# Optimization experiments

Measured on AMD Instinct MI355X. Metric: run time of the kernel, lower is better.

## Reference

```python
import jax, jax.numpy as jnp
import numpy as np

BS, D_IN, D_OUT, N_MASKS = 1024, 512, 512, 8

def setup_inputs() -> dict:
    key = jax.random.key(0)
    k1, k2, k3, k4 = jax.random.split(key, 4)
    x = jax.random.normal(k1, (BS, D_IN), dtype=jnp.float32)
    state = jax.random.randint(k2, (BS,), 0, N_MASKS, dtype=jnp.int32)
    # glorot-uniform-like kernel
    limit = float(np.sqrt(6.0 / (D_IN + D_OUT)))
    kernel = jax.random.uniform(k3, (D_IN, D_OUT), dtype=jnp.float32, minval=-limit, maxval=limit)
    # binary MADE connectivity masks (0/1)
    masks = (jax.random.uniform(k4, (N_MASKS, D_IN, D_OUT)) < 0.5).astype(jnp.float32)
    return {"x": x, "state": state, "kernel": kernel, "masks": masks}

def reference(x, state, kernel, masks):
    # Math of original: out = relu(x[b] @ (kernel * masks[state[b]]))
    # Efficient form: precompute all n masked kernels (small n), batched matmul,
    # then gather per-sample result. Avoids materializing [bs, d_in, d_out].
    masked = kernel[None, :, :] * masks            # [n, d_in, d_out]
    y_all = jnp.einsum('bi,nio->bno', x, masked)   # [bs, n, d_out]
    y = jnp.take_along_axis(y_all, state[:, None, None].astype(jnp.int32), axis=1)[:, 0, :]
    return jax.nn.relu(y)
```

## Files before the change

### kernel.cpp

```cpp
#include <hip/hip_runtime.h>

#define BS 1024
#define D_IN 512
#define D_OUT 512
#define N_MASKS 8

typedef short bf16x8 __attribute__((ext_vector_type(8)));
typedef float f32x4 __attribute__((ext_vector_type(4)));

#define WF_OFF_USH (8192 / 2)
#define WF_USH     (N_MASKS * 16 * 32 * 512)
#define XB_OFF_USH (WF_OFF_USH + WF_USH)

__device__ __forceinline__ ushort f2bf(float f) {
    union { float f; unsigned u; } x; x.f = f;
    unsigned r = (x.u + 0x7fffu + ((x.u >> 16) & 1u)) >> 16;
    return (ushort)r;
}

__global__ void __launch_bounds__(256) prep_kernel(
    const float* __restrict__ x, const int* __restrict__ state,
    const float* __restrict__ kern, const float* __restrict__ masks,
    int* __restrict__ wsi, ushort* __restrict__ wf, ushort* __restrict__ xb)
{
    const int bx  = blockIdx.x;
    const int tid = threadIdx.x;

    if (bx < 1024) {
        const int n  = bx >> 7;
        const int kb = (bx >> 3) & 15;
        const int cb = (bx & 7) * 4 + (tid >> 6);
        const int l  = tid & 63;
        const int g  = l >> 4;
        const int cl = l & 15;
        const int k0  = kb * 32 + g * 8;
        const int col = cb * 16 + cl;
        const float* kp = kern + (size_t)k0 * D_OUT + col;
        const float* mp = masks + (size_t)n * (D_IN * D_OUT) + (size_t)k0 * D_OUT + col;
        uint pk[4];
        #pragma unroll
        for (int j = 0; j < 4; ++j) {
            float v0 = kp[(2*j)   * D_OUT] * mp[(2*j)   * D_OUT];
            float v1 = kp[(2*j+1) * D_OUT] * mp[(2*j+1) * D_OUT];
            pk[j] = (uint)f2bf(v0) | ((uint)f2bf(v1) << 16);
        }
        uint4 o; o.x = pk[0]; o.y = pk[1]; o.z = pk[2]; o.w = pk[3];
        *(uint4*)(wf + ((size_t)((n * 16 + kb) * 32 + cb)) * 512 + l * 8) = o;
    } else if (bx < 1280) {
        const int idx = (bx - 1024) * 256 + tid;
        const float4 a = ((const float4*)x)[idx * 2];
        const float4 b = ((const float4*)x)[idx * 2 + 1];
        uint4 o;
        o.x = (uint)f2bf(a.x) | ((uint)f2bf(a.y) << 16);
        o.y = (uint)f2bf(a.z) | ((uint)f2bf(a.w) << 16);
        o.z = (uint)f2bf(b.x) | ((uint)f2bf(b.y) << 16);
        o.w = (uint)f2bf(b.z) | ((uint)f2bf(b.w) << 16);
        *(uint4*)(xb + (size_t)idx * 8) = o;
    } else {
        __shared__ int cnt[N_MASKS];
        __shared__ int offs[N_MASKS + 1];
        if (tid < N_MASKS) cnt[tid] = 0;
        __syncthreads();
        int s[4];
        #pragma unroll
        for (int r = 0; r < 4; ++r) {
            s[r] = state[r * 256 + tid];
            atomicAdd(&cnt[s[r]], 1);
        }
        __syncthreads();
        if (tid == 0) {
            int acc = 0;
            for (int i = 0; i < N_MASKS; ++i) { offs[i] = acc; acc += cnt[i]; }
            offs[N_MASKS] = acc;
        }
        __syncthreads();
        if (tid <= N_MASKS) wsi[tid] = offs[tid];
        if (tid < N_MASKS) cnt[tid] = offs[tid];
        __syncthreads();
        #pragma unroll
        for (int r = 0; r < 4; ++r) {
            const int pos = atomicAdd(&cnt[s[r]], 1);
            wsi[16 + pos] = r * 256 + tid;
        }
    }
}

__global__ void __launch_bounds__(256) gemm_kernel(
    const ushort* __restrict__ xb, const ushort* __restrict__ wf,
    const int* __restrict__ wsi, float* __restrict__ out)
{
    const int n     = blockIdx.x;
    const int cb128 = blockIdx.y;
    const int rt    = blockIdx.z;

    const int off0 = wsi[n];
    const int off1 = wsi[n + 1];
    if (rt * 16 >= off1 - off0) return;

    __shared__ int ridx[16];
    const int tid = threadIdx.x;
    if (tid < 16) {
        const int p = off0 + rt * 16 + tid;
        ridx[tid] = (p < off1) ? wsi[16 + p] : -1;
    }
    __syncthreads();

    const int lane = tid & 63;
    const int wid  = tid >> 6;
    const int g    = lane >> 4;
    const int cl   = lane & 15;

    const int myrow = ridx[cl];
    const ushort* xrow = xb + (size_t)(myrow < 0 ? 0 : myrow) * D_IN + g * 8;
    const int cb0 = cb128 * 8 + wid * 2;
    const ushort* wp = wf + ((size_t)(n * 16) * 32 + cb0) * 512 + lane * 8;

    f32x4 acc0 = {0.f, 0.f, 0.f, 0.f};
    f32x4 acc1 = {0.f, 0.f, 0.f, 0.f};

    #pragma unroll
    for (int kb = 0; kb < 16; ++kb) {
        const bf16x8 a  = *(const bf16x8*)(xrow + kb * 32);
        const bf16x8 b0 = *(const bf16x8*)(wp + (size_t)kb * 32 * 512);
        const bf16x8 b1 = *(const bf16x8*)(wp + (size_t)kb * 32 * 512 + 512);
        acc0 = __builtin_amdgcn_mfma_f32_16x16x32_bf16(a, b0, acc0, 0, 0, 0);
        acc1 = __builtin_amdgcn_mfma_f32_16x16x32_bf16(a, b1, acc1, 0, 0, 0);
    }

    #pragma unroll
    for (int r = 0; r < 4; ++r) {
        const int b = ridx[g * 4 + r];
        if (b >= 0) {
            float* op = out + (size_t)b * D_OUT;
            op[cb0 * 16 + cl]       = fmaxf(acc0[r], 0.f);
            op[(cb0 + 1) * 16 + cl] = fmaxf(acc1[r], 0.f);
        }
    }
}

extern "C" void kernel_launch(void* const* d_in, const int* in_sizes, int n_in,
                              void* d_out, int out_size, void* d_ws, size_t ws_size,
                              hipStream_t stream) {
    const float* x     = (const float*)d_in[0];
    const int*   state = (const int*)d_in[1];
    const float* kern  = (const float*)d_in[2];
    const float* masks = (const float*)d_in[3];
    float*  out = (float*)d_out;
    int*    wsi = (int*)d_ws;
    ushort* wsu = (ushort*)d_ws;

    prep_kernel<<<1281, 256, 0, stream>>>(x, state, kern, masks,
                                          wsi, wsu + WF_OFF_USH, wsu + XB_OFF_USH);
    dim3 grid(N_MASKS, D_OUT / 128, BS / 16);
    gemm_kernel<<<grid, 256, 0, stream>>>(wsu + XB_OFF_USH, wsu + WF_OFF_USH, wsi, out);
}
```

Before: 17.87 us.

## Transpose masked weights via LDS staging for coalesced prep and k-contiguous GEMM reads

New measurement: 23.50 us. 31.5% more time.

```diff
diff --git a/kernel.cpp b/kernel.cpp
--- a/kernel.cpp
+++ b/kernel.cpp
@@ -9,7 +9,7 @@
 typedef float f32x4 __attribute__((ext_vector_type(4)));
 
 #define WF_OFF_USH (8192 / 2)
-#define WF_USH     (N_MASKS * 16 * 32 * 512)
+#define WF_USH     (N_MASKS * D_OUT * D_IN)
 #define XB_OFF_USH (WF_OFF_USH + WF_USH)
 
 __device__ __forceinline__ ushort f2bf(float f) {
@@ -23,31 +23,48 @@
     const float* __restrict__ kern, const float* __restrict__ masks,
     int* __restrict__ wsi, ushort* __restrict__ wf, ushort* __restrict__ xb)
 {
+    __shared__ float prod[32][132];
     const int bx  = blockIdx.x;
     const int tid = threadIdx.x;
 
-    if (bx < 1024) {
-        const int n  = bx >> 7;
-        const int kb = (bx >> 3) & 15;
-        const int cb = (bx & 7) * 4 + (tid >> 6);
-        const int l  = tid & 63;
-        const int g  = l >> 4;
-        const int cl = l & 15;
-        const int k0  = kb * 32 + g * 8;
-        const int col = cb * 16 + cl;
-        const float* kp = kern + (size_t)k0 * D_OUT + col;
-        const float* mp = masks + (size_t)n * (D_IN * D_OUT) + (size_t)k0 * D_OUT + col;
-        uint pk[4];
+    if (bx < 512) {
+        const int n  = bx >> 6;
+        const int kb = (bx >> 2) & 15;
+        const int cg = bx & 3;
+        const int k0 = kb * 32, c0 = cg * 128;
+        const float* maskn = masks + (size_t)n * (D_IN * D_OUT);
+
         #pragma unroll
-        for (int j = 0; j < 4; ++j) {
-            float v0 = kp[(2*j)   * D_OUT] * mp[(2*j)   * D_OUT];
-            float v1 = kp[(2*j+1) * D_OUT] * mp[(2*j+1) * D_OUT];
-            pk[j] = (uint)f2bf(v0) | ((uint)f2bf(v1) << 16);
+        for (int it = 0; it < 4; ++it) {
+            const int i  = it * 256 + tid;
+            const int r  = i >> 5;
+            const int c4 = i & 31;
+            const size_t g = (size_t)(k0 + r) * D_OUT + c0 + c4 * 4;
+            const float4 kv = *(const float4*)&kern[g];
+            const float4 mv = *(const float4*)&maskn[g];
+            float* dst = &prod[r][c4 * 4];
+            dst[0] = kv.x * mv.x; dst[1] = kv.y * mv.y;
+            dst[2] = kv.z * mv.z; dst[3] = kv.w * mv.w;
         }
-        uint4 o; o.x = pk[0]; o.y = pk[1]; o.z = pk[2]; o.w = pk[3];
-        *(uint4*)(wf + ((size_t)((n * 16 + kb) * 32 + cb)) * 512 + l * 8) = o;
-    } else if (bx < 1280) {
-        const int idx = (bx - 1024) * 256 + tid;
+        __syncthreads();
+
+        #pragma unroll
+        for (int it = 0; it < 2; ++it) {
+            const int c = it * 64 + (tid >> 2);
+            const int q = tid & 3;
+            uint4 o;
+            uint pk[4];
+            #pragma unroll
+            for (int h = 0; h < 4; ++h) {
+                const float v0 = prod[q * 8 + 2 * h][c];
+                const float v1 = prod[q * 8 + 2 * h + 1][c];
+                pk[h] = (uint)f2bf(v0) | ((uint)f2bf(v1) << 16);
+            }
+            o.x = pk[0]; o.y = pk[1]; o.z = pk[2]; o.w = pk[3];
+            *(uint4*)(wf + ((size_t)(n * D_OUT) + c0 + c) * D_IN + k0 + q * 8) = o;
+        }
+    } else if (bx < 768) {
+        const int idx = (bx - 512) * 256 + tid;
         const float4 a = ((const float4*)x)[idx * 2];
         const float4 b = ((const float4*)x)[idx * 2 + 1];
         uint4 o;
@@ -89,9 +106,8 @@
     const ushort* __restrict__ xb, const ushort* __restrict__ wf,
     const int* __restrict__ wsi, float* __restrict__ out)
 {
-    const int n     = blockIdx.x;
-    const int cb128 = blockIdx.y;
-    const int rt    = blockIdx.z;
+    const int n  = blockIdx.x;
+    const int rt = blockIdx.z;
 
     const int off0 = wsi[n];
     const int off1 = wsi[n + 1];
@@ -112,8 +128,9 @@
 
     const int myrow = ridx[cl];
     const ushort* xrow = xb + (size_t)(myrow < 0 ? 0 : myrow) * D_IN + g * 8;
-    const int cb0 = cb128 * 8 + wid * 2;
-    const ushort* wp = wf + ((size_t)(n * 16) * 32 + cb0) * 512 + lane * 8;
+    const int cf0 = blockIdx.y * 8 + wid * 2;
+    const ushort* wp0 = wf + ((size_t)(n * D_OUT) + cf0 * 16 + cl) * D_IN + g * 8;
+    const ushort* wp1 = wp0 + 16 * D_IN;
 
     f32x4 acc0 = {0.f, 0.f, 0.f, 0.f};
     f32x4 acc1 = {0.f, 0.f, 0.f, 0.f};
@@ -121,8 +138,8 @@
     #pragma unroll
     for (int kb = 0; kb < 16; ++kb) {
         const bf16x8 a  = *(const bf16x8*)(xrow + kb * 32);
-        const bf16x8 b0 = *(const bf16x8*)(wp + (size_t)kb * 32 * 512);
-        const bf16x8 b1 = *(const bf16x8*)(wp + (size_t)kb * 32 * 512 + 512);
+        const bf16x8 b0 = *(const bf16x8*)(wp0 + kb * 32);
+        const bf16x8 b1 = *(const bf16x8*)(wp1 + kb * 32);
         acc0 = __builtin_amdgcn_mfma_f32_16x16x32_bf16(a, b0, acc0, 0, 0, 0);
         acc1 = __builtin_amdgcn_mfma_f32_16x16x32_bf16(a, b1, acc1, 0, 0, 0);
     }
@@ -132,8 +149,8 @@
         const int b = ridx[g * 4 + r];
         if (b >= 0) {
             float* op = out + (size_t)b * D_OUT;
-            op[cb0 * 16 + cl]       = fmaxf(acc0[r], 0.f);
-            op[(cb0 + 1) * 16 + cl] = fmaxf(acc1[r], 0.f);
+            op[cf0 * 16 + cl]       = fmaxf(acc0[r], 0.f);
+            op[(cf0 + 1) * 16 + cl] = fmaxf(acc1[r], 0.f);
         }
     }
 }
@@ -149,8 +166,8 @@
     int*    wsi = (int*)d_ws;
     ushort* wsu = (ushort*)d_ws;
 
-    prep_kernel<<<1281, 256, 0, stream>>>(x, state, kern, masks,
-                                          wsi, wsu + WF_OFF_USH, wsu + XB_OFF_USH);
+    prep_kernel<<<769, 256, 0, stream>>>(x, state, kern, masks,
+                                         wsi, wsu + WF_OFF_USH, wsu + XB_OFF_USH);
     dim3 grid(N_MASKS, D_OUT / 128, BS / 16);
     gemm_kernel<<<grid, 256, 0, stream>>>(wsu + XB_OFF_USH, wsu + WF_OFF_USH, wsi, out);
 }
```

## Split K across waves with LDS reduction and grid-stride row tiles

Applied to the files above, without the earlier changes.

Measured after the change: 15.89 us. 1.12x faster.

```diff
diff --git a/kernel.cpp b/kernel.cpp
--- a/kernel.cpp
+++ b/kernel.cpp
@@ -85,56 +85,64 @@
     }
 }
 
-__global__ void __launch_bounds__(256) gemm_kernel(
+__global__ void __launch_bounds__(256, 4) gemm_kernel(
     const ushort* __restrict__ xb, const ushort* __restrict__ wf,
     const int* __restrict__ wsi, float* __restrict__ out)
 {
-    const int n     = blockIdx.x;
-    const int cb128 = blockIdx.y;
-    const int rt    = blockIdx.z;
-
+    const int n   = blockIdx.x;
+    const int cb0 = blockIdx.y * 2;
     const int off0 = wsi[n];
     const int off1 = wsi[n + 1];
-    if (rt * 16 >= off1 - off0) return;
+    const int gcnt = off1 - off0;
 
-    __shared__ int ridx[16];
-    const int tid = threadIdx.x;
-    if (tid < 16) {
-        const int p = off0 + rt * 16 + tid;
-        ridx[tid] = (p < off1) ? wsi[16 + p] : -1;
-    }
-    __syncthreads();
-
+    const int tid  = threadIdx.x;
     const int lane = tid & 63;
     const int wid  = tid >> 6;
     const int g    = lane >> 4;
     const int cl   = lane & 15;
 
-    const int myrow = ridx[cl];
-    const ushort* xrow = xb + (size_t)(myrow < 0 ? 0 : myrow) * D_IN + g * 8;
-    const int cb0 = cb128 * 8 + wid * 2;
-    const ushort* wp = wf + ((size_t)(n * 16) * 32 + cb0) * 512 + lane * 8;
+    __shared__ float red[3][2][64][4];
 
-    f32x4 acc0 = {0.f, 0.f, 0.f, 0.f};
-    f32x4 acc1 = {0.f, 0.f, 0.f, 0.f};
+    const ushort* wp0 = wf + ((size_t)((n * 16 + wid * 4) * 32 + cb0)) * 512 + lane * 8;
 
-    #pragma unroll
-    for (int kb = 0; kb < 16; ++kb) {
-        const bf16x8 a  = *(const bf16x8*)(xrow + kb * 32);
-        const bf16x8 b0 = *(const bf16x8*)(wp + (size_t)kb * 32 * 512);
-        const bf16x8 b1 = *(const bf16x8*)(wp + (size_t)kb * 32 * 512 + 512);
-        acc0 = __builtin_amdgcn_mfma_f32_16x16x32_bf16(a, b0, acc0, 0, 0, 0);
-        acc1 = __builtin_amdgcn_mfma_f32_16x16x32_bf16(a, b1, acc1, 0, 0, 0);
-    }
+    for (int rt = blockIdx.z; rt * 16 < gcnt; rt += 8) {
+        const int p  = off0 + rt * 16 + cl;
+        const int rv = (p < off1) ? wsi[16 + p] : -1;
+        const ushort* xr = xb + (size_t)(rv < 0 ? 0 : rv) * D_IN + wid * 4 * 32 + g * 8;
 
-    #pragma unroll
-    for (int r = 0; r < 4; ++r) {
-        const int b = ridx[g * 4 + r];
-        if (b >= 0) {
-            float* op = out + (size_t)b * D_OUT;
-            op[cb0 * 16 + cl]       = fmaxf(acc0[r], 0.f);
-            op[(cb0 + 1) * 16 + cl] = fmaxf(acc1[r], 0.f);
+        f32x4 acc0 = {0.f, 0.f, 0.f, 0.f};
+        f32x4 acc1 = {0.f, 0.f, 0.f, 0.f};
+        #pragma unroll
+        for (int i = 0; i < 4; ++i) {
+            const bf16x8 a  = *(const bf16x8*)(xr + i * 32);
+            const bf16x8 b0 = *(const bf16x8*)(wp0 + (size_t)i * 32 * 512);
+            const bf16x8 b1 = *(const bf16x8*)(wp0 + (size_t)i * 32 * 512 + 512);
+            acc0 = __builtin_amdgcn_mfma_f32_16x16x32_bf16(a, b0, acc0, 0, 0, 0);
+            acc1 = __builtin_amdgcn_mfma_f32_16x16x32_bf16(a, b1, acc1, 0, 0, 0);
         }
+
+        if (wid) {
+            *(f32x4*)&red[wid - 1][0][lane][0] = acc0;
+            *(f32x4*)&red[wid - 1][1][lane][0] = acc1;
+        }
+        __syncthreads();
+        if (wid == 0) {
+            #pragma unroll
+            for (int w = 0; w < 3; ++w) {
+                acc0 += *(const f32x4*)&red[w][0][lane][0];
+                acc1 += *(const f32x4*)&red[w][1][lane][0];
+            }
+            #pragma unroll
+            for (int r = 0; r < 4; ++r) {
+                const int brow = __shfl(rv, g * 4 + r);
+                if (brow >= 0) {
+                    float* op = out + (size_t)brow * D_OUT;
+                    op[cb0 * 16 + cl]       = fmaxf(acc0[r], 0.f);
+                    op[(cb0 + 1) * 16 + cl] = fmaxf(acc1[r], 0.f);
+                }
+            }
+        }
+        __syncthreads();
     }
 }
 
@@ -151,6 +159,6 @@
 
     prep_kernel<<<1281, 256, 0, stream>>>(x, state, kern, masks,
                                           wsi, wsu + WF_OFF_USH, wsu + XB_OFF_USH);
-    dim3 grid(N_MASKS, D_OUT / 128, BS / 16);
+    dim3 grid(N_MASKS, 16, 8);
     gemm_kernel<<<grid, 256, 0, stream>>>(wsu + XB_OFF_USH, wsu + WF_OFF_USH, wsi, out);
 }
```
